# Kernel tuning notes

Measured on AMD Instinct MI355X. Metric: run time of the kernel, lower is better.

Reference implementation:

```python
import jax, jax.numpy as jnp
import numpy as np

B, D, L = 8, 512, 8192


def log_g(x):
    # th.where(x >= 0, log(relu(x) + 1), x)
    return jnp.where(x >= 0, jnp.log1p(jnp.maximum(x, 0.0)), x)


def min_gru(hg):
    # hg: [B, H, L] -> [B, H/2, L]
    h, gate = jnp.split(hg, 2, axis=1)
    log_coeffs = -jax.nn.softplus(gate)                      # log a_t
    log_values = -jax.nn.softplus(-gate) + log_g(h)          # log b_t
    a_star = jnp.cumsum(log_coeffs, axis=2)
    log_h0_plus_b_star = jax.lax.cumlogsumexp(log_values - a_star, axis=2)
    return jnp.exp(a_star + log_h0_plus_b_star)


def conv1x1(x, w, b):
    # x: [B, D, L], w: [E, D], b: [E]  (kernel-size-1 Conv1d == pointwise linear)
    return jnp.einsum('ed,bdl->bel', w, x) + b[None, :, None]


def setup_inputs() -> dict:
    key = jax.random.key(0)
    k1, k2, k3, k4, k5 = jax.random.split(key, 5)
    scale = 1.0 / np.sqrt(D)
    x = jax.random.normal(k1, (B, D, L), dtype=jnp.float32)
    w_fore = jax.random.normal(k2, (D, D), dtype=jnp.float32) * scale
    b_fore = jax.random.normal(k3, (D,), dtype=jnp.float32) * scale
    w_back = jax.random.normal(k4, (D, D), dtype=jnp.float32) * scale
    b_back = jax.random.normal(k5, (D,), dtype=jnp.float32) * scale
    return {'x': x, 'w_fore': w_fore, 'b_fore': b_fore, 'w_back': w_back, 'b_back': b_back}


def reference(x, w_fore, b_fore, w_back, b_back):
    fore = min_gru(conv1x1(x, w_fore, b_fore))                            # [B, D/2, L]
    back = jnp.flip(min_gru(conv1x1(jnp.flip(x, 2), w_back, b_back)), 2)  # [B, D/2, L]
    return jnp.concatenate([fore, back], axis=1)                          # [B, D, L]
```

## Files before the change

kernel.cpp:

```cpp
#include <hip/hip_runtime.h>

#define BATCH 8
#define DIN   512
#define SEQ   8192
#define ECH   1024
#define HCH   256
#define CL    32
#define NCHNK (SEQ / CL)

typedef __bf16 bf16;
typedef __bf16 bf16x8 __attribute__((ext_vector_type(8)));
typedef __bf16 bf16x4 __attribute__((ext_vector_type(4)));
typedef float  floatx4 __attribute__((ext_vector_type(4)));

__device__ __forceinline__ void async_ld16(void* lds, const void* g) {
  __builtin_amdgcn_global_load_lds(
      (const __attribute__((address_space(1))) unsigned int*)g,
      (__attribute__((address_space(3))) unsigned int*)lds, 16, 0, 0);
}

__device__ __forceinline__ float bits2f(unsigned u) {
  return __builtin_bit_cast(float, u);
}

__global__ void k_wconv(const float* __restrict__ wf, const float* __restrict__ bfo,
                        const float* __restrict__ wb, const float* __restrict__ bb,
                        bf16* __restrict__ Wb, float* __restrict__ bias) {
  int idx = blockIdx.x * 256 + threadIdx.x;
  if (idx < ECH * DIN) {
    int n = idx >> 9, d = idx & 511;
    int dir = n >> 9, r = n & 511, e = r >> 1, isg = r & 1;
    int s = e + (isg ? HCH : 0);
    const float* w = dir ? wb : wf;
    Wb[idx] = (bf16)w[s * DIN + d];
  }
  if (idx < ECH) {
    int dir = idx >> 9, r = idx & 511, e = r >> 1, isg = r & 1;
    int s = e + (isg ? HCH : 0);
    bias[idx] = (dir ? bb : bfo)[s];
  }
}

__global__ void k_xpose(const float* __restrict__ x, bf16* __restrict__ xT) {
  __shared__ float T[64 * 65];
  int t = threadIdx.x;
  int l0 = blockIdx.x * 64;
  int d0 = blockIdx.y * 64;
  int b  = blockIdx.z;
  const float* xb = x + (size_t)b * DIN * SEQ;
#pragma unroll
  for (int p = 0; p < 4; ++p) {
    int dl = (t >> 4) + p * 16;
    int l4 = (t & 15) * 4;
    float4 v = *(const float4*)(xb + (size_t)(d0 + dl) * SEQ + l0 + l4);
    T[dl * 65 + l4 + 0] = v.x;
    T[dl * 65 + l4 + 1] = v.y;
    T[dl * 65 + l4 + 2] = v.z;
    T[dl * 65 + l4 + 3] = v.w;
  }
  __syncthreads();
  bf16* xTb = xT + (size_t)b * SEQ * DIN;
#pragma unroll
  for (int p = 0; p < 4; ++p) {
    int ll = (t >> 4) + p * 16;
    int d4 = (t & 15) * 4;
    bf16x4 h;
#pragma unroll
    for (int j = 0; j < 4; ++j) h[j] = (bf16)T[(d4 + j) * 65 + ll];
    *(bf16x4*)(xTb + (size_t)(l0 + ll) * DIN + d0 + d4) = h;
  }
}

__launch_bounds__(256, 2)
__global__ void k_gemm(const bf16* __restrict__ xT, const bf16* __restrict__ Wb,
                       const float* __restrict__ bias, bf16* __restrict__ hg) {
  __shared__ bf16 lds[16384];
  bf16* As = lds;
  bf16* Bs = lds + 8192;

  int t = threadIdx.x;
  int lane = t & 63, wave = t >> 6;
  int n0 = blockIdx.x * 128;
  int l0 = blockIdx.y * 128;
  int b  = blockIdx.z;
  int l15 = lane & 15, quad = lane >> 4;
  int wm = wave >> 1, wn = wave & 1;
  int mb = wm * 64, nb = wn * 64;

  const bf16* gA = xT + ((size_t)b * SEQ + l0) * DIN;
  const bf16* gB = Wb + (size_t)n0 * DIN;

  int srow = wave * 32 + (lane >> 3);
  int scol = (lane & 7) * 8;

  floatx4 acc[4][4];
#pragma unroll
  for (int i = 0; i < 4; ++i)
#pragma unroll
    for (int j = 0; j < 4; ++j) acc[i][j] = (floatx4){0.f, 0.f, 0.f, 0.f};

  for (int kt = 0; kt < DIN / 64; ++kt) {
    int k0 = kt * 64;
#pragma unroll
    for (int q = 0; q < 4; ++q) {
      async_ld16(As + (wave * 32 + q * 8) * 64,
                 gA + (size_t)(srow + q * 8) * DIN + k0 + scol);
      async_ld16(Bs + (wave * 32 + q * 8) * 64,
                 gB + (size_t)(srow + q * 8) * DIN + k0 + scol);
    }
    __syncthreads();
#pragma unroll
    for (int kk = 0; kk < 64; kk += 32) {
      bf16x8 af[4], bfr[4];
#pragma unroll
      for (int i = 0; i < 4; ++i)
        af[i] = *(const bf16x8*)(As + (mb + i * 16 + l15) * 64 + kk + quad * 8);
#pragma unroll
      for (int i = 0; i < 4; ++i)
        bfr[i] = *(const bf16x8*)(Bs + (nb + i * 16 + l15) * 64 + kk + quad * 8);
#pragma unroll
      for (int mi = 0; mi < 4; ++mi)
#pragma unroll
        for (int ni = 0; ni < 4; ++ni)
          acc[mi][ni] = __builtin_amdgcn_mfma_f32_16x16x32_bf16(
              af[mi], bfr[ni], acc[mi][ni], 0, 0, 0);
    }
    __syncthreads();
  }

  float bb4[4];
#pragma unroll
  for (int ni = 0; ni < 4; ++ni) bb4[ni] = bias[n0 + nb + ni * 16 + l15];
  bf16* Cs = lds;
#pragma unroll
  for (int mi = 0; mi < 4; ++mi)
#pragma unroll
    for (int ni = 0; ni < 4; ++ni)
#pragma unroll
      for (int r = 0; r < 4; ++r) {
        int row = mb + mi * 16 + quad * 4 + r;
        int col = nb + ni * 16 + l15;
        Cs[row * 128 + col] = (bf16)(acc[mi][ni][r] + bb4[ni]);
      }
  __syncthreads();
  bf16* hgb = hg + ((size_t)b * SEQ + l0) * ECH + n0;
#pragma unroll
  for (int p = 0; p < 8; ++p) {
    int row = p * 16 + (t >> 4);
    int seg = t & 15;
    *(bf16x8*)(hgb + (size_t)row * ECH + seg * 8) =
        *(const bf16x8*)(Cs + row * 128 + seg * 8);
  }
}

__device__ __forceinline__ void gru_ab(unsigned v, float& a, float& bt) {
  float hh = bits2f(v << 16);
  float g  = bits2f(v & 0xffff0000u);
  float eg = __expf(-g);
  float sg = 1.f / (1.f + eg);
  a = eg * sg;
  float gv = hh >= 0.f ? 1.f + hh : __expf(hh);
  bt = sg * gv;
}

__global__ void k_scan1(const bf16* __restrict__ hg, float* __restrict__ Asum,
                        float* __restrict__ Bsum) {
  int t = threadIdx.x;
  int chunk = blockIdx.x, dir = blockIdx.y, b = blockIdx.z;
  const bf16* hb = hg + (size_t)b * SEQ * ECH + dir * 512 + 2 * t;
  float A = 1.f, Bc = 0.f;
  int lbase = chunk * CL;
#pragma unroll 8
  for (int i = 0; i < CL; ++i) {
    int l = dir ? (lbase + CL - 1 - i) : (lbase + i);
    unsigned v = *(const unsigned*)(hb + (size_t)l * ECH);
    float a, bt;
    gru_ab(v, a, bt);
    A *= a;
    Bc = a * Bc + bt;
  }
  size_t o = ((size_t)(b * 2 + dir) * NCHNK + chunk) * 256 + t;
  Asum[o] = A;
  Bsum[o] = Bc;
}

__global__ void k_scan2(const float* __restrict__ Asum, const float* __restrict__ Bsum,
                        float* __restrict__ hin) {
  int tid = blockIdx.x * 256 + threadIdx.x;
  int b = tid >> 9, dir = (tid >> 8) & 1, e = tid & 255;
  size_t rb = (size_t)(b * 2 + dir) * NCHNK;
  float h = 0.f;
  if (dir == 0) {
    for (int c = 0; c < NCHNK; ++c) {
      size_t o = (rb + c) * 256 + e;
      hin[o] = h;
      h = Asum[o] * h + Bsum[o];
    }
  } else {
    for (int c = NCHNK - 1; c >= 0; --c) {
      size_t o = (rb + c) * 256 + e;
      hin[o] = h;
      h = Asum[o] * h + Bsum[o];
    }
  }
}

__global__ void k_scan3(const bf16* __restrict__ hg, const float* __restrict__ hin,
                        float* __restrict__ out) {
  __shared__ float T[256 * 33];
  int t = threadIdx.x;
  int chunk = blockIdx.x, dir = blockIdx.y, b = blockIdx.z;
  const bf16* hb = hg + (size_t)b * SEQ * ECH + dir * 512 + 2 * t;
  float h = hin[((size_t)(b * 2 + dir) * NCHNK + chunk) * 256 + t];
  int lbase = chunk * CL;
#pragma unroll 8
  for (int i = 0; i < CL; ++i) {
    int ll = dir ? (CL - 1 - i) : i;
    unsigned v = *(const unsigned*)(hb + (size_t)(lbase + ll) * ECH);
    float a, bt;
    gru_ab(v, a, bt);
    h = a * h + bt;
    T[t * 33 + ll] = h;
  }
  __syncthreads();
  float* ob = out + ((size_t)b * 512 + dir * 256) * SEQ + lbase;
#pragma unroll
  for (int p = 0; p < 8; ++p) {
    int row = p * 32 + (t >> 3);
    int c4 = (t & 7) * 4;
    float4 v4;
    v4.x = T[row * 33 + c4 + 0];
    v4.y = T[row * 33 + c4 + 1];
    v4.z = T[row * 33 + c4 + 2];
    v4.w = T[row * 33 + c4 + 3];
    *(float4*)(ob + (size_t)row * SEQ + c4) = v4;
  }
}

extern "C" void kernel_launch(void* const* d_in, const int* in_sizes, int n_in,
                              void* d_out, int out_size, void* d_ws, size_t ws_size,
                              hipStream_t stream) {
  const float* x   = (const float*)d_in[0];
  const float* wf  = (const float*)d_in[1];
  const float* bfo = (const float*)d_in[2];
  const float* wb  = (const float*)d_in[3];
  const float* bb  = (const float*)d_in[4];
  float* out = (float*)d_out;
  char* ws = (char*)d_ws;

  bf16*  xT   = (bf16*)(ws);
  bf16*  hg   = (bf16*)(ws + 67108864);
  bf16*  Wbm  = (bf16*)(ws + 201326592);
  float* bias = (float*)(ws + 202375168);
  float* Asum = (float*)(ws + 202379264);
  float* Bsum = (float*)(ws + 206573568);
  float* hin  = (float*)(ws + 210767872);

  k_wconv<<<2048, 256, 0, stream>>>(wf, bfo, wb, bb, Wbm, bias);
  k_xpose<<<dim3(SEQ / 64, DIN / 64, BATCH), 256, 0, stream>>>(x, xT);
  k_gemm<<<dim3(ECH / 128, SEQ / 128, BATCH), 256, 0, stream>>>(xT, Wbm, bias, hg);
  k_scan1<<<dim3(NCHNK, 2, BATCH), 256, 0, stream>>>(hg, Asum, Bsum);
  k_scan2<<<16, 256, 0, stream>>>(Asum, Bsum, hin);
  k_scan3<<<dim3(NCHNK, 2, BATCH), 256, 0, stream>>>(hg, hin, out);
}
```

Before: 412.6 us.

## Parallelize chunk-carry scan, swizzle GEMM LDS, remap tiles per XCD, widen transpose stores

The serial 256-step chunk-carry scan, which ran on only 16 blocks, is split into three stages: 16 super-chunks reduced in parallel, a short 16-step serial scan, and a parallel expansion back to per-chunk carries. The GEMM gains an XOR swizzle on LDS columns to avoid bank conflicts, a padded output staging stride, and a block-index remap so that tiles sharing rows of xT land on the same XCD. The transpose kernel writes 16-byte bf16x8 stores instead of 8-byte ones. The cost is two extra kernel launches and a little extra workspace.

```diff
diff --git a/kernel.cpp b/kernel.cpp
--- a/kernel.cpp
+++ b/kernel.cpp
@@ -7,6 +7,7 @@
 #define HCH   256
 #define CL    32
 #define NCHNK (SEQ / CL)
+#define NSC   16
 
 typedef __bf16 bf16;
 typedef __bf16 bf16x8 __attribute__((ext_vector_type(8)));
@@ -61,28 +62,35 @@
   __syncthreads();
   bf16* xTb = xT + (size_t)b * SEQ * DIN;
 #pragma unroll
-  for (int p = 0; p < 4; ++p) {
-    int ll = (t >> 4) + p * 16;
-    int d4 = (t & 15) * 4;
-    bf16x4 h;
-#pragma unroll
-    for (int j = 0; j < 4; ++j) h[j] = (bf16)T[(d4 + j) * 65 + ll];
-    *(bf16x4*)(xTb + (size_t)(l0 + ll) * DIN + d0 + d4) = h;
+  for (int p = 0; p < 2; ++p) {
+    int ll = (t >> 3) + p * 32;
+    int d8 = (t & 7) * 8;
+    bf16x8 h;
+#pragma unroll
+    for (int j = 0; j < 8; ++j) h[j] = (bf16)T[(d8 + j) * 65 + ll];
+    *(bf16x8*)(xTb + (size_t)(l0 + ll) * DIN + d0 + d8) = h;
   }
 }
 
 __launch_bounds__(256, 2)
 __global__ void k_gemm(const bf16* __restrict__ xT, const bf16* __restrict__ Wb,
                        const float* __restrict__ bias, bf16* __restrict__ hg) {
-  __shared__ bf16 lds[16384];
+  __shared__ bf16 lds[16896];
   bf16* As = lds;
   bf16* Bs = lds + 8192;
 
   int t = threadIdx.x;
   int lane = t & 63, wave = t >> 6;
-  int n0 = blockIdx.x * 128;
-  int l0 = blockIdx.y * 128;
+
+  int lin = blockIdx.x + 8 * blockIdx.y;
+  int xcd = lin & 7;
+  int seq = lin >> 3;
+  int ltile = xcd + 8 * (seq >> 3);
+  int ntile = seq & 7;
+  int n0 = ntile * 128;
+  int l0 = ltile * 128;
   int b  = blockIdx.z;
+
   int l15 = lane & 15, quad = lane >> 4;
   int wm = wave >> 1, wn = wave & 1;
   int mb = wm * 64, nb = wn * 64;
@@ -91,7 +99,7 @@
   const bf16* gB = Wb + (size_t)n0 * DIN;
 
   int srow = wave * 32 + (lane >> 3);
-  int scol = (lane & 7) * 8;
+  int scol = (((lane & 7) ^ (lane >> 3)) * 8);
 
   floatx4 acc[4][4];
 #pragma unroll
@@ -111,13 +119,16 @@
     __syncthreads();
 #pragma unroll
     for (int kk = 0; kk < 64; kk += 32) {
+      int rsw = l15 & 7;
       bf16x8 af[4], bfr[4];
 #pragma unroll
       for (int i = 0; i < 4; ++i)
-        af[i] = *(const bf16x8*)(As + (mb + i * 16 + l15) * 64 + kk + quad * 8);
+        af[i] = *(const bf16x8*)(As + (mb + i * 16 + l15) * 64 +
+                                 (((kk >> 3) + quad) ^ rsw) * 8);
 #pragma unroll
       for (int i = 0; i < 4; ++i)
-        bfr[i] = *(const bf16x8*)(Bs + (nb + i * 16 + l15) * 64 + kk + quad * 8);
+        bfr[i] = *(const bf16x8*)(Bs + (nb + i * 16 + l15) * 64 +
+                                  (((kk >> 3) + quad) ^ rsw) * 8);
 #pragma unroll
       for (int mi = 0; mi < 4; ++mi)
 #pragma unroll
@@ -140,7 +151,7 @@
       for (int r = 0; r < 4; ++r) {
         int row = mb + mi * 16 + quad * 4 + r;
         int col = nb + ni * 16 + l15;
-        Cs[row * 128 + col] = (bf16)(acc[mi][ni][r] + bb4[ni]);
+        Cs[row * 132 + col] = (bf16)(acc[mi][ni][r] + bb4[ni]);
       }
   __syncthreads();
   bf16* hgb = hg + ((size_t)b * SEQ + l0) * ECH + n0;
@@ -149,7 +160,7 @@
     int row = p * 16 + (t >> 4);
     int seg = t & 15;
     *(bf16x8*)(hgb + (size_t)row * ECH + seg * 8) =
-        *(const bf16x8*)(Cs + row * 128 + seg * 8);
+        *(const bf16x8*)(Cs + row * 132 + seg * 8);
   }
 }
 
@@ -184,24 +195,46 @@
   Bsum[o] = Bc;
 }
 
-__global__ void k_scan2(const float* __restrict__ Asum, const float* __restrict__ Bsum,
-                        float* __restrict__ hin) {
-  int tid = blockIdx.x * 256 + threadIdx.x;
-  int b = tid >> 9, dir = (tid >> 8) & 1, e = tid & 255;
-  size_t rb = (size_t)(b * 2 + dir) * NCHNK;
+__global__ void k_scan2a(const float* __restrict__ Asum, const float* __restrict__ Bsum,
+                         float* __restrict__ SA, float* __restrict__ SB) {
+  int e = threadIdx.x, sc = blockIdx.x, row2 = blockIdx.y, dir = row2 & 1;
+  size_t base = (size_t)row2 * NCHNK;
+  float Acc = 1.f, Bcc = 0.f;
+#pragma unroll
+  for (int i = 0; i < 16; ++i) {
+    int c = sc * 16 + (dir ? 15 - i : i);
+    size_t o = (base + c) * 256 + e;
+    float a = Asum[o], bv = Bsum[o];
+    Acc = a * Acc;
+    Bcc = a * Bcc + bv;
+  }
+  size_t so = ((size_t)row2 * NSC + sc) * 256 + e;
+  SA[so] = Acc;
+  SB[so] = Bcc;
+}
+
+__global__ void k_scan2b(const float* __restrict__ SA, const float* __restrict__ SB,
+                         float* __restrict__ hsc) {
+  int e = threadIdx.x, row2 = blockIdx.x, dir = row2 & 1;
   float h = 0.f;
-  if (dir == 0) {
-    for (int c = 0; c < NCHNK; ++c) {
-      size_t o = (rb + c) * 256 + e;
-      hin[o] = h;
-      h = Asum[o] * h + Bsum[o];
-    }
-  } else {
-    for (int c = NCHNK - 1; c >= 0; --c) {
-      size_t o = (rb + c) * 256 + e;
-      hin[o] = h;
-      h = Asum[o] * h + Bsum[o];
-    }
+  for (int i = 0; i < NSC; ++i) {
+    int sc = dir ? NSC - 1 - i : i;
+    size_t o = ((size_t)row2 * NSC + sc) * 256 + e;
+    hsc[o] = h;
+    h = SA[o] * h + SB[o];
+  }
+}
+
+__global__ void k_scan2c(const float* __restrict__ Asum, const float* __restrict__ Bsum,
+                         const float* __restrict__ hsc, float* __restrict__ hin) {
+  int e = threadIdx.x, sc = blockIdx.x, row2 = blockIdx.y, dir = row2 & 1;
+  float h = hsc[((size_t)row2 * NSC + sc) * 256 + e];
+#pragma unroll
+  for (int i = 0; i < 16; ++i) {
+    int c = sc * 16 + (dir ? 15 - i : i);
+    size_t o = ((size_t)row2 * NCHNK + c) * 256 + e;
+    hin[o] = h;
+    h = Asum[o] * h + Bsum[o];
   }
 }
 
@@ -255,11 +288,16 @@
   float* Asum = (float*)(ws + 202379264);
   float* Bsum = (float*)(ws + 206573568);
   float* hin  = (float*)(ws + 210767872);
+  float* SA   = (float*)(ws + 214962176);
+  float* SB   = (float*)(ws + 215224320);
+  float* hsc  = (float*)(ws + 215486464);
 
   k_wconv<<<2048, 256, 0, stream>>>(wf, bfo, wb, bb, Wbm, bias);
   k_xpose<<<dim3(SEQ / 64, DIN / 64, BATCH), 256, 0, stream>>>(x, xT);
   k_gemm<<<dim3(ECH / 128, SEQ / 128, BATCH), 256, 0, stream>>>(xT, Wbm, bias, hg);
   k_scan1<<<dim3(NCHNK, 2, BATCH), 256, 0, stream>>>(hg, Asum, Bsum);
-  k_scan2<<<16, 256, 0, stream>>>(Asum, Bsum, hin);
+  k_scan2a<<<dim3(NSC, 16), 256, 0, stream>>>(Asum, Bsum, SA, SB);
+  k_scan2b<<<16, 256, 0, stream>>>(SA, SB, hsc);
+  k_scan2c<<<dim3(NSC, 16), 256, 0, stream>>>(Asum, Bsum, hsc, hin);
   k_scan3<<<dim3(NCHNK, 2, BATCH), 256, 0, stream>>>(hg, hin, out);
 }
```

Measured after the change: 387.3 us. 1.07x faster.
